# Kernel tuning notes

Measured on AMD Instinct MI355X. Metric: run time of the kernel, lower is better.

## Reference

```python
import jax, jax.numpy as jnp
import numpy as np

DIM = 1024
HEADS = 16
DIM_HEAD = 64
INNER = HEADS * DIM_HEAD
EPS_NORM = 1e-12  # F.normalize eps
LN_EPS = 1e-5     # torch F.layer_norm default eps


def setup_inputs() -> dict:
    key = jax.random.key(0)
    ks = jax.random.split(key, 6)
    x = jax.random.normal(ks[0], (8, 1024, DIM), dtype=jnp.float32)
    ln_gamma = jnp.ones((DIM,), jnp.float32)
    q_gamma = jnp.ones((HEADS, 1, DIM_HEAD), jnp.float32)
    k_gamma = jnp.ones((HEADS, 1, DIM_HEAD), jnp.float32)
    # nn.Linear default init ~ U(-1/sqrt(fan_in), 1/sqrt(fan_in))
    w_qkv = jax.random.uniform(ks[1], (DIM, 3 * INNER), jnp.float32, -1.0, 1.0) / np.sqrt(DIM)
    w_out = jax.random.uniform(ks[2], (INNER, DIM), jnp.float32, -1.0, 1.0) / np.sqrt(INNER)
    return {"x": x, "ln_gamma": ln_gamma, "q_gamma": q_gamma, "k_gamma": k_gamma,
            "w_qkv": w_qkv, "w_out": w_out}


def _layer_norm(x, gamma):
    mu = jnp.mean(x, axis=-1, keepdims=True)
    var = jnp.var(x, axis=-1, keepdims=True)
    return (x - mu) * jax.lax.rsqrt(var + LN_EPS) * gamma  # beta is zeros buffer


def _rms(x, gamma):
    # F.normalize(x, dim=-1) * sqrt(d) * gamma
    n = jnp.linalg.norm(x, axis=-1, keepdims=True)
    normed = x / jnp.maximum(n, EPS_NORM)
    return normed * (DIM_HEAD ** 0.5) * gamma


def reference(x, ln_gamma, q_gamma, k_gamma, w_qkv, w_out):
    b, n, _ = x.shape
    h, d = HEADS, DIM_HEAD
    xn = _layer_norm(x, ln_gamma)
    qkv = xn @ w_qkv  # [b, n, 3*inner]
    q, k, v = jnp.split(qkv, 3, axis=-1)
    # b n (h d) -> b h n d
    to_heads = lambda t: t.reshape(b, n, h, d).transpose(0, 2, 1, 3)
    q, k, v = to_heads(q), to_heads(k), to_heads(v)
    q = _rms(q, q_gamma)
    k = _rms(k, k_gamma)
    dots = jnp.einsum('bhid,bhjd->bhij', q, k)  # no extra scale (scale baked into RMSNorm)
    attn = jax.nn.softmax(dots, axis=-1)
    out = jnp.einsum('bhij,bhjd->bhid', attn, v)
    out = out.transpose(0, 2, 1, 3).reshape(b, n, h * d)
    return out @ w_out
```

## Files before the change

### kernel.cpp

```cpp
#include <hip/hip_runtime.h>
#include <hip/hip_bf16.h>
#include <math.h>

#define DIMX   1024
#define HEADS  16
#define DH     64
#define NB     8
#define NSEQ   1024
#define ROWS   (NB * NSEQ)
#define QKVW   (3 * DIMX)

typedef _Float16 half8 __attribute__((ext_vector_type(8)));
typedef _Float16 half4 __attribute__((ext_vector_type(4)));
typedef float floatx4 __attribute__((ext_vector_type(4)));

#define GLD_LDS16(gptr, lptr) __builtin_amdgcn_global_load_lds( \
    (const __attribute__((address_space(1))) void*)(gptr),      \
    (__attribute__((address_space(3))) void*)(lptr), 16, 0, 0)

__global__ __launch_bounds__(256) void ln_kernel(const float* __restrict__ x,
                                                 const float* __restrict__ gamma,
                                                 _Float16* __restrict__ xn) {
    int row = blockIdx.x;
    const float* xr = x + (size_t)row * DIMX;
    _Float16* xo = xn + (size_t)row * DIMX;
    int t = threadIdx.x;

    float4 v = ((const float4*)xr)[t];
    float s  = v.x + v.y + v.z + v.w;
    float ss = v.x*v.x + v.y*v.y + v.z*v.z + v.w*v.w;

    #pragma unroll
    for (int o = 32; o > 0; o >>= 1) {
        s  += __shfl_down(s, o);
        ss += __shfl_down(ss, o);
    }
    __shared__ float sbuf[4], ssbuf[4];
    int lane = t & 63, wid = t >> 6;
    if (lane == 0) { sbuf[wid] = s; ssbuf[wid] = ss; }
    __syncthreads();
    if (t == 0) {
        float a = 0.f, b2 = 0.f;
        for (int i = 0; i < 4; i++) { a += sbuf[i]; b2 += ssbuf[i]; }
        sbuf[0] = a; ssbuf[0] = b2;
    }
    __syncthreads();
    float mean = sbuf[0] * (1.0f / DIMX);
    float var  = ssbuf[0] * (1.0f / DIMX) - mean * mean;
    float rstd = rsqrtf(var + 1e-5f);

    float4 g = ((const float4*)gamma)[t];
    half4 o;
    o.x = (_Float16)((v.x - mean) * rstd * g.x);
    o.y = (_Float16)((v.y - mean) * rstd * g.y);
    o.z = (_Float16)((v.z - mean) * rstd * g.z);
    o.w = (_Float16)((v.w - mean) * rstd * g.w);
    *(half4*)(xo + t * 4) = o;
}

__global__ __launch_bounds__(256) void wtrans(const float* __restrict__ W,
                                              _Float16* __restrict__ WT,
                                              int K, int N) {
    __shared__ float tile[32][33];
    int n0 = blockIdx.x * 32, k0 = blockIdx.y * 32;
    int tx = threadIdx.x & 31, ty = threadIdx.x >> 5;
    #pragma unroll
    for (int i = 0; i < 32; i += 8)
        tile[ty + i][tx] = W[(size_t)(k0 + ty + i) * N + n0 + tx];
    __syncthreads();
    #pragma unroll
    for (int i = 0; i < 32; i += 8)
        WT[(size_t)(n0 + ty + i) * K + k0 + tx] = (_Float16)tile[tx][ty + i];
}

template <typename CT>
__global__ __launch_bounds__(256) void hgemm(const _Float16* __restrict__ A,
                                             const _Float16* __restrict__ BT,
                                             CT* __restrict__ C,
                                             int M, int N, int K) {
    __shared__ _Float16 As[128 * 64];
    __shared__ _Float16 Bs[128 * 64];

    int t = threadIdx.x;
    int wave = t >> 6, lane = t & 63;
    int quad = lane >> 4, l16 = lane & 15;
    int wm = (wave >> 1) * 64, wn = (wave & 1) * 64;
    size_t m0 = (size_t)blockIdx.y * 128, n0 = (size_t)blockIdx.x * 128;

    floatx4 acc[4][4] = {};

    int sr = t >> 3, sg = t & 7;
    int swz = sg ^ (sr & 7);
    const _Float16* ag = A  + (m0 + sr) * (size_t)K + swz * 8;
    const _Float16* bg = BT + (n0 + sr) * (size_t)K + swz * 8;
    char* lA = (char*)As + (t >> 6) * 1024;
    char* lB = (char*)Bs + (t >> 6) * 1024;

    for (int k0 = 0; k0 < K; k0 += 64) {
        #pragma unroll
        for (int i = 0; i < 4; i++) {
            GLD_LDS16(ag + (size_t)(i * 32) * K + k0, lA + i * 4096);
            GLD_LDS16(bg + (size_t)(i * 32) * K + k0, lB + i * 4096);
        }
        __syncthreads();

        half8 af[2][4], bf[2][4];
        #pragma unroll
        for (int kk = 0; kk < 2; kk++) {
            #pragma unroll
            for (int mf = 0; mf < 4; mf++)
                af[kk][mf] = *(const half8*)&As[(wm + mf * 16 + l16) * 64
                                 + (((kk * 4 + quad) ^ (l16 & 7)) * 8)];
            #pragma unroll
            for (int nf = 0; nf < 4; nf++)
                bf[kk][nf] = *(const half8*)&Bs[(wn + nf * 16 + l16) * 64
                                 + (((kk * 4 + quad) ^ (l16 & 7)) * 8)];
        }

        #pragma unroll
        for (int kk = 0; kk < 2; kk++)
            #pragma unroll
            for (int mf = 0; mf < 4; mf++)
                #pragma unroll
                for (int nf = 0; nf < 4; nf++)
                    acc[mf][nf] = __builtin_amdgcn_mfma_f32_16x16x32_f16(
                        af[kk][mf], bf[kk][nf], acc[mf][nf], 0, 0, 0);
        __syncthreads();
    }

    #pragma unroll
    for (int mf = 0; mf < 4; mf++)
        #pragma unroll
        for (int nf = 0; nf < 4; nf++)
            #pragma unroll
            for (int r = 0; r < 4; r++) {
                size_t row = m0 + wm + mf * 16 + quad * 4 + r;
                size_t col = n0 + wn + nf * 16 + l16;
                C[row * N + col] = (CT)acc[mf][nf][r];
            }
}

__global__ __launch_bounds__(256) void rmsvt(const _Float16* __restrict__ qkv,
                                             const float* __restrict__ qg,
                                             const float* __restrict__ kg,
                                             _Float16* __restrict__ qf,
                                             _Float16* __restrict__ kf,
                                             _Float16* __restrict__ vt) {
    __shared__ _Float16 tile[64][72];
    int blk = blockIdx.x;
    int bh = blk >> 4, nt = blk & 15;
    int b = bh >> 4, h = bh & 15;
    int t = threadIdx.x;
    int r = t >> 2, cg = t & 3;

    const _Float16* src = qkv + ((size_t)(b * NSEQ) + nt * 64 + r) * QKVW + h * 64 + cg * 16;
    size_t drow = ((size_t)bh * 1024 + nt * 64 + r) * 64 + cg * 16;

    half8 q0 = *(const half8*)(src);
    half8 q1 = *(const half8*)(src + 8);
    float sq = 0.f;
    #pragma unroll
    for (int j = 0; j < 8; j++) { float a=(float)q0[j], b2=(float)q1[j]; sq += a*a + b2*b2; }
    sq += __shfl_xor(sq, 1); sq += __shfl_xor(sq, 2);
    float qs = 8.0f / fmaxf(sqrtf(sq), 1e-12f);
    half8 oq0, oq1;
    #pragma unroll
    for (int j = 0; j < 8; j++) {
        oq0[j] = (_Float16)((float)q0[j] * qs * qg[h * 64 + cg * 16 + j]);
        oq1[j] = (_Float16)((float)q1[j] * qs * qg[h * 64 + cg * 16 + 8 + j]);
    }
    *(half8*)(qf + drow) = oq0;
    *(half8*)(qf + drow + 8) = oq1;

    half8 k0 = *(const half8*)(src + DIMX);
    half8 k1 = *(const half8*)(src + DIMX + 8);
    float sk = 0.f;
    #pragma unroll
    for (int j = 0; j < 8; j++) { float a=(float)k0[j], b2=(float)k1[j]; sk += a*a + b2*b2; }
    sk += __shfl_xor(sk, 1); sk += __shfl_xor(sk, 2);
    float ks = 8.0f / fmaxf(sqrtf(sk), 1e-12f);
    half8 ok0, ok1;
    #pragma unroll
    for (int j = 0; j < 8; j++) {
        ok0[j] = (_Float16)((float)k0[j] * ks * kg[h * 64 + cg * 16 + j]);
        ok1[j] = (_Float16)((float)k1[j] * ks * kg[h * 64 + cg * 16 + 8 + j]);
    }
    *(half8*)(kf + drow) = ok0;
    *(half8*)(kf + drow + 8) = ok1;

    half8 v0 = *(const half8*)(src + 2 * DIMX);
    half8 v1 = *(const half8*)(src + 2 * DIMX + 8);
    #pragma unroll
    for (int j = 0; j < 8; j++) tile[cg * 16 + j][r] = v0[j];
    #pragma unroll
    for (int j = 0; j < 8; j++) tile[cg * 16 + 8 + j][r] = v1[j];
    __syncthreads();
    int d = t >> 2, ng = t & 3;
    half8 w0, w1;
    #pragma unroll
    for (int j = 0; j < 8; j++) { w0[j] = tile[d][ng * 16 + j]; w1[j] = tile[d][ng * 16 + 8 + j]; }
    _Float16* vdst = vt + ((size_t)blk * 64 + d) * 64 + ng * 16;
    *(half8*)vdst = w0;
    *(half8*)(vdst + 8) = w1;
}

__global__ __launch_bounds__(256) void flash_kernel(const _Float16* __restrict__ qf,
                                                    const _Float16* __restrict__ kf,
                                                    const _Float16* __restrict__ vt,
                                                    _Float16* __restrict__ obuf) {
    __shared__ _Float16 Ks[64 * 64];
    __shared__ _Float16 VTs[64 * 64];
    __shared__ _Float16 Ps[4][16][72];

    int t = threadIdx.x;
    int wave = t >> 6, lane = t & 63;
    int quad = lane >> 4, l16 = lane & 15;
    int bh = blockIdx.x >> 3, qt = blockIdx.x & 7;

    const _Float16* qb = qf + ((size_t)bh * 1024 + qt * 128) * 64;
    const _Float16* kb = kf + (size_t)bh * 65536;
    const _Float16* vb = vt + (size_t)bh * 65536;

    half8 aq[2][2];
    #pragma unroll
    for (int st = 0; st < 2; st++) {
        const _Float16* qrow = qb + (wave * 32 + st * 16 + l16) * 64;
        aq[st][0] = *(const half8*)(qrow + quad * 8);
        aq[st][1] = *(const half8*)(qrow + 32 + quad * 8);
    }

    floatx4 o[2][4] = {};
    float m_i[2] = {-INFINITY, -INFINITY};
    float l_i[2] = {0.f, 0.f};

    int sr = t >> 3;
    int sg = t & 7;
    int swz = sg ^ (sr & 7);
    char* lK = (char*)Ks  + (t >> 6) * 1024;
    char* lV = (char*)VTs + (t >> 6) * 1024;

    for (int kt = 0; kt < 16; kt++) {
        const _Float16* kbt = kb + (size_t)kt * 64 * 64;
        const _Float16* vbt = vb + (size_t)kt * 64 * 64;
        #pragma unroll
        for (int i = 0; i < 2; i++) {
            GLD_LDS16(kbt + (i * 32 + sr) * 64 + swz * 8, lK + i * 4096);
            GLD_LDS16(vbt + (i * 32 + sr) * 64 + swz * 8, lV + i * 4096);
        }
        __syncthreads();

        #pragma unroll
        for (int st = 0; st < 2; st++) {
            floatx4 sc[4] = {};
            #pragma unroll
            for (int kc = 0; kc < 2; kc++) {
                #pragma unroll
                for (int nf = 0; nf < 4; nf++) {
                    half8 ak = *(const half8*)&Ks[(nf * 16 + l16) * 64
                                    + (((kc * 4 + quad) ^ (l16 & 7)) * 8)];
                    sc[nf] = __builtin_amdgcn_mfma_f32_16x16x32_f16(
                        ak, aq[st][kc], sc[nf], 0, 0, 0);
                }
            }

            float mx = sc[0][0];
            #pragma unroll
            for (int nf = 0; nf < 4; nf++)
                #pragma unroll
                for (int r = 0; r < 4; r++) mx = fmaxf(mx, sc[nf][r]);
            mx = fmaxf(mx, __shfl_xor(mx, 16));
            mx = fmaxf(mx, __shfl_xor(mx, 32));
            float mnew = fmaxf(m_i[st], mx);
            float alpha = __expf(m_i[st] - mnew);
            m_i[st] = mnew;
            float psum = 0.f;
            #pragma unroll
            for (int nf = 0; nf < 4; nf++)
                #pragma unroll
                for (int r = 0; r < 4; r++) {
                    float p = __expf(sc[nf][r] - mnew);
                    sc[nf][r] = p;
                    psum += p;
                }
            l_i[st] = l_i[st] * alpha + psum;
            #pragma unroll
            for (int nf = 0; nf < 4; nf++) o[st][nf] *= alpha;

            #pragma unroll
            for (int nf = 0; nf < 4; nf++) {
                half4 p4;
                #pragma unroll
                for (int r = 0; r < 4; r++) p4[r] = (_Float16)sc[nf][r];
                *(half4*)&Ps[wave][l16][nf * 16 + quad * 4] = p4;
            }

            #pragma unroll
            for (int kc = 0; kc < 2; kc++) {
                half8 bp = *(const half8*)&Ps[wave][l16][kc * 32 + quad * 8];
                #pragma unroll
                for (int nf = 0; nf < 4; nf++) {
                    half8 av = *(const half8*)&VTs[(nf * 16 + l16) * 64
                                    + (((kc * 4 + quad) ^ (l16 & 7)) * 8)];
                    o[st][nf] = __builtin_amdgcn_mfma_f32_16x16x32_f16(
                        av, bp, o[st][nf], 0, 0, 0);
                }
            }
        }
        __syncthreads();
    }

    int b = bh >> 4, h = bh & 15;
    #pragma unroll
    for (int st = 0; st < 2; st++) {
        float lsum = l_i[st];
        lsum += __shfl_xor(lsum, 16);
        lsum += __shfl_xor(lsum, 32);
        float inv = 1.0f / lsum;
        size_t row = (size_t)b * NSEQ + qt * 128 + wave * 32 + st * 16 + l16;
        #pragma unroll
        for (int nf = 0; nf < 4; nf++) {
            half4 o4;
            #pragma unroll
            for (int r = 0; r < 4; r++) o4[r] = (_Float16)(o[st][nf][r] * inv);
            *(half4*)(obuf + row * 1024 + h * 64 + nf * 16 + quad * 4) = o4;
        }
    }
}

extern "C" void kernel_launch(void* const* d_in, const int* in_sizes, int n_in,
                              void* d_out, int out_size, void* d_ws, size_t ws_size,
                              hipStream_t stream) {
    const float* x     = (const float*)d_in[0];
    const float* ln_g  = (const float*)d_in[1];
    const float* q_g   = (const float*)d_in[2];
    const float* k_g   = (const float*)d_in[3];
    const float* w_qkv = (const float*)d_in[4];
    const float* w_out = (const float*)d_in[5];
    float* out = (float*)d_out;

    char* base = (char*)d_ws;
    _Float16* xn    = (_Float16*)(base);
    _Float16* obuf  = (_Float16*)(base);
    _Float16* qkv   = (_Float16*)(base + (16ull << 20));
    _Float16* wqkvT = (_Float16*)(base + (64ull << 20));
    _Float16* woutT = (_Float16*)(base + (72ull << 20));
    _Float16* qf    = (_Float16*)(base + (80ull << 20));
    _Float16* kf    = (_Float16*)(base + (96ull << 20));
    _Float16* vt    = (_Float16*)(base + (112ull << 20));

    ln_kernel<<<ROWS, 256, 0, stream>>>(x, ln_g, xn);

    dim3 gt1(QKVW / 32, DIMX / 32);
    wtrans<<<gt1, 256, 0, stream>>>(w_qkv, wqkvT, DIMX, QKVW);

    dim3 g1(QKVW / 128, ROWS / 128);
    hgemm<_Float16><<<g1, 256, 0, stream>>>(xn, wqkvT, qkv, ROWS, QKVW, DIMX);

    rmsvt<<<NB * HEADS * (NSEQ / 64), 256, 0, stream>>>(qkv, q_g, k_g, qf, kf, vt);

    dim3 gt2(DIMX / 32, DIMX / 32);
    wtrans<<<gt2, 256, 0, stream>>>(w_out, woutT, DIMX, DIMX);

    flash_kernel<<<NB * HEADS * (NSEQ / 128), 256, 0, stream>>>(qf, kf, vt, obuf);

    dim3 g2(DIMX / 128, ROWS / 128);
    hgemm<float><<<g2, 256, 0, stream>>>(obuf, woutT, out, ROWS, DIMX, DIMX);
}
```

Before: 288.7 us.

## Fuse q/k RMS norm into QKV GEMM epilogue, merge weight transposes, use exp2 softmax

The QKV GEMM now swaps its MFMA operands so each lane holds a token row, and applies the q/k RMS normalization and head-major scatter in its epilogue. This removes the full fp16 qkv buffer round trip and the separate rmsvt pass. Only a small V-transpose kernel remains. The two weight transposes are merged into one launch, and the softmax switches to exp2 with log2e folded into q, rescaling lazily only when the row max grows. The output GEMM writes float4 vectors, and the P staging buffer padding is changed. The cost is more register pressure in the GEMM epilogue and divergent branches in the softmax.

```diff
diff --git a/kernel.cpp b/kernel.cpp
--- a/kernel.cpp
+++ b/kernel.cpp
@@ -9,6 +9,7 @@
 #define NSEQ   1024
 #define ROWS   (NB * NSEQ)
 #define QKVW   (3 * DIMX)
+#define LOG2E  1.44269504088896f
 
 typedef _Float16 half8 __attribute__((ext_vector_type(8)));
 typedef _Float16 half4 __attribute__((ext_vector_type(4)));
@@ -17,6 +18,14 @@
 #define GLD_LDS16(gptr, lptr) __builtin_amdgcn_global_load_lds( \
     (const __attribute__((address_space(1))) void*)(gptr),      \
     (__attribute__((address_space(3))) void*)(lptr), 16, 0, 0)
+
+__device__ __forceinline__ float fexp2(float x) {
+#if __has_builtin(__builtin_amdgcn_exp2f)
+    return __builtin_amdgcn_exp2f(x);
+#else
+    return __expf(x * 0.69314718056f);
+#endif
+}
 
 __global__ __launch_bounds__(256) void ln_kernel(const float* __restrict__ x,
                                                  const float* __restrict__ gamma,
@@ -58,11 +67,15 @@
     *(half4*)(xo + t * 4) = o;
 }
 
-__global__ __launch_bounds__(256) void wtrans(const float* __restrict__ W,
-                                              _Float16* __restrict__ WT,
-                                              int K, int N) {
+__global__ __launch_bounds__(256) void wtrans2(const float* __restrict__ Wq,
+                                               const float* __restrict__ Wo,
+                                               _Float16* __restrict__ WqT,
+                                               _Float16* __restrict__ WoT) {
     __shared__ float tile[32][33];
-    int n0 = blockIdx.x * 32, k0 = blockIdx.y * 32;
+    const float* W; _Float16* WT; int N, n0;
+    if (blockIdx.x < 96) { W = Wq; WT = WqT; N = QKVW; n0 = blockIdx.x * 32; }
+    else                 { W = Wo; WT = WoT; N = DIMX; n0 = (blockIdx.x - 96) * 32; }
+    int k0 = blockIdx.y * 32;
     int tx = threadIdx.x & 31, ty = threadIdx.x >> 5;
     #pragma unroll
     for (int i = 0; i < 32; i += 8)
@@ -70,21 +83,25 @@
     __syncthreads();
     #pragma unroll
     for (int i = 0; i < 32; i += 8)
-        WT[(size_t)(n0 + ty + i) * K + k0 + tx] = (_Float16)tile[tx][ty + i];
-}
-
-template <typename CT>
-__global__ __launch_bounds__(256) void hgemm(const _Float16* __restrict__ A,
-                                             const _Float16* __restrict__ BT,
-                                             CT* __restrict__ C,
-                                             int M, int N, int K) {
+        WT[(size_t)(n0 + ty + i) * 1024 + k0 + tx] = (_Float16)tile[tx][ty + i];
+}
+
+__global__ __launch_bounds__(256) void hgemm_qkv(const _Float16* __restrict__ A,
+                                                 const _Float16* __restrict__ BT,
+                                                 const float* __restrict__ qg,
+                                                 const float* __restrict__ kg,
+                                                 _Float16* __restrict__ qf,
+                                                 _Float16* __restrict__ kf,
+                                                 _Float16* __restrict__ vraw) {
     __shared__ _Float16 As[128 * 64];
     __shared__ _Float16 Bs[128 * 64];
+    const int K = DIMX;
 
     int t = threadIdx.x;
     int wave = t >> 6, lane = t & 63;
     int quad = lane >> 4, l16 = lane & 15;
-    int wm = (wave >> 1) * 64, wn = (wave & 1) * 64;
+    int wm = (wave >> 1) * 64;
+    int wn = (wave & 1) * 64;
     size_t m0 = (size_t)blockIdx.y * 128, n0 = (size_t)blockIdx.x * 128;
 
     floatx4 acc[4][4] = {};
@@ -124,72 +141,63 @@
                 #pragma unroll
                 for (int nf = 0; nf < 4; nf++)
                     acc[mf][nf] = __builtin_amdgcn_mfma_f32_16x16x32_f16(
-                        af[kk][mf], bf[kk][nf], acc[mf][nf], 0, 0, 0);
-        __syncthreads();
-    }
-
-    #pragma unroll
-    for (int mf = 0; mf < 4; mf++)
-        #pragma unroll
-        for (int nf = 0; nf < 4; nf++)
-            #pragma unroll
-            for (int r = 0; r < 4; r++) {
-                size_t row = m0 + wm + mf * 16 + quad * 4 + r;
-                size_t col = n0 + wn + nf * 16 + l16;
-                C[row * N + col] = (CT)acc[mf][nf][r];
-            }
-}
-
-__global__ __launch_bounds__(256) void rmsvt(const _Float16* __restrict__ qkv,
-                                             const float* __restrict__ qg,
-                                             const float* __restrict__ kg,
-                                             _Float16* __restrict__ qf,
-                                             _Float16* __restrict__ kf,
-                                             _Float16* __restrict__ vt) {
+                        bf[kk][nf], af[kk][mf], acc[mf][nf], 0, 0, 0);
+        __syncthreads();
+    }
+
+    int which = (int)(n0 >> 10);
+    int nloc  = ((int)n0 & 1023) + wn;
+    int h = nloc >> 6;
+    const float* g = (which == 0) ? qg : kg;
+    float emul = (which == 0) ? LOG2E : 1.0f;
+    _Float16* dstbuf = (which == 0) ? qf : (which == 1) ? kf : vraw;
+
+    #pragma unroll
+    for (int mf = 0; mf < 4; mf++) {
+        size_t tok = m0 + wm + mf * 16 + l16;
+        int b = (int)(tok >> 10), ntk = (int)(tok & 1023);
+        _Float16* dst = dstbuf + (((size_t)(b * 16 + h)) * 1024 + ntk) * 64;
+        if (which < 2) {
+            float ss = 0.f;
+            #pragma unroll
+            for (int nf = 0; nf < 4; nf++)
+                #pragma unroll
+                for (int r = 0; r < 4; r++) ss += acc[mf][nf][r] * acc[mf][nf][r];
+            ss += __shfl_xor(ss, 16);
+            ss += __shfl_xor(ss, 32);
+            float scale = 8.0f * emul / fmaxf(sqrtf(ss), 1e-12f);
+            #pragma unroll
+            for (int nf = 0; nf < 4; nf++) {
+                half4 p;
+                #pragma unroll
+                for (int r = 0; r < 4; r++)
+                    p[r] = (_Float16)(acc[mf][nf][r] * scale *
+                                      g[h * 64 + nf * 16 + quad * 4 + r]);
+                *(half4*)(dst + nf * 16 + quad * 4) = p;
+            }
+        } else {
+            #pragma unroll
+            for (int nf = 0; nf < 4; nf++) {
+                half4 p;
+                #pragma unroll
+                for (int r = 0; r < 4; r++) p[r] = (_Float16)acc[mf][nf][r];
+                *(half4*)(dst + nf * 16 + quad * 4) = p;
+            }
+        }
+    }
+}
+
+__global__ __launch_bounds__(256) void vtrans(const _Float16* __restrict__ vraw,
+                                              _Float16* __restrict__ vt) {
     __shared__ _Float16 tile[64][72];
     int blk = blockIdx.x;
     int bh = blk >> 4, nt = blk & 15;
-    int b = bh >> 4, h = bh & 15;
     int t = threadIdx.x;
     int r = t >> 2, cg = t & 3;
 
-    const _Float16* src = qkv + ((size_t)(b * NSEQ) + nt * 64 + r) * QKVW + h * 64 + cg * 16;
-    size_t drow = ((size_t)bh * 1024 + nt * 64 + r) * 64 + cg * 16;
-
-    half8 q0 = *(const half8*)(src);
-    half8 q1 = *(const half8*)(src + 8);
-    float sq = 0.f;
-    #pragma unroll
-    for (int j = 0; j < 8; j++) { float a=(float)q0[j], b2=(float)q1[j]; sq += a*a + b2*b2; }
-    sq += __shfl_xor(sq, 1); sq += __shfl_xor(sq, 2);
-    float qs = 8.0f / fmaxf(sqrtf(sq), 1e-12f);
-    half8 oq0, oq1;
-    #pragma unroll
-    for (int j = 0; j < 8; j++) {
-        oq0[j] = (_Float16)((float)q0[j] * qs * qg[h * 64 + cg * 16 + j]);
-        oq1[j] = (_Float16)((float)q1[j] * qs * qg[h * 64 + cg * 16 + 8 + j]);
-    }
-    *(half8*)(qf + drow) = oq0;
-    *(half8*)(qf + drow + 8) = oq1;
-
-    half8 k0 = *(const half8*)(src + DIMX);
-    half8 k1 = *(const half8*)(src + DIMX + 8);
-    float sk = 0.f;
-    #pragma unroll
-    for (int j = 0; j < 8; j++) { float a=(float)k0[j], b2=(float)k1[j]; sk += a*a + b2*b2; }
-    sk += __shfl_xor(sk, 1); sk += __shfl_xor(sk, 2);
-    float ks = 8.0f / fmaxf(sqrtf(sk), 1e-12f);
-    half8 ok0, ok1;
-    #pragma unroll
-    for (int j = 0; j < 8; j++) {
-        ok0[j] = (_Float16)((float)k0[j] * ks * kg[h * 64 + cg * 16 + j]);
-        ok1[j] = (_Float16)((float)k1[j] * ks * kg[h * 64 + cg * 16 + 8 + j]);
-    }
-    *(half8*)(kf + drow) = ok0;
-    *(half8*)(kf + drow + 8) = ok1;
-
-    half8 v0 = *(const half8*)(src + 2 * DIMX);
-    half8 v1 = *(const half8*)(src + 2 * DIMX + 8);
+    const _Float16* src = vraw + ((size_t)bh * 1024 + nt * 64 + r) * 64 + cg * 16;
+    half8 v0 = *(const half8*)src;
+    half8 v1 = *(const half8*)(src + 8);
     #pragma unroll
     for (int j = 0; j < 8; j++) tile[cg * 16 + j][r] = v0[j];
     #pragma unroll
@@ -210,7 +218,7 @@
                                                     _Float16* __restrict__ obuf) {
     __shared__ _Float16 Ks[64 * 64];
     __shared__ _Float16 VTs[64 * 64];
-    __shared__ _Float16 Ps[4][16][72];
+    __shared__ _Float16 Ps[4][16][68];
 
     int t = threadIdx.x;
     int wave = t >> 6, lane = t & 63;
@@ -270,21 +278,24 @@
                 for (int r = 0; r < 4; r++) mx = fmaxf(mx, sc[nf][r]);
             mx = fmaxf(mx, __shfl_xor(mx, 16));
             mx = fmaxf(mx, __shfl_xor(mx, 32));
-            float mnew = fmaxf(m_i[st], mx);
-            float alpha = __expf(m_i[st] - mnew);
-            m_i[st] = mnew;
+            if (mx > m_i[st]) {
+                float alpha = fexp2(m_i[st] - mx);
+                l_i[st] *= alpha;
+                #pragma unroll
+                for (int nf = 0; nf < 4; nf++) o[st][nf] *= alpha;
+                m_i[st] = mx;
+            }
+            float mcur = m_i[st];
             float psum = 0.f;
             #pragma unroll
             for (int nf = 0; nf < 4; nf++)
                 #pragma unroll
                 for (int r = 0; r < 4; r++) {
-                    float p = __expf(sc[nf][r] - mnew);
+                    float p = fexp2(sc[nf][r] - mcur);
                     sc[nf][r] = p;
                     psum += p;
                 }
-            l_i[st] = l_i[st] * alpha + psum;
-            #pragma unroll
-            for (int nf = 0; nf < 4; nf++) o[st][nf] *= alpha;
+            l_i[st] += psum;
 
             #pragma unroll
             for (int nf = 0; nf < 4; nf++) {
@@ -296,7 +307,11 @@
 
             #pragma unroll
             for (int kc = 0; kc < 2; kc++) {
-                half8 bp = *(const half8*)&Ps[wave][l16][kc * 32 + quad * 8];
+                half4 p0 = *(const half4*)&Ps[wave][l16][kc * 32 + quad * 8];
+                half4 p1 = *(const half4*)&Ps[wave][l16][kc * 32 + quad * 8 + 4];
+                half8 bp;
+                #pragma unroll
+                for (int j = 0; j < 4; j++) { bp[j] = p0[j]; bp[4 + j] = p1[j]; }
                 #pragma unroll
                 for (int nf = 0; nf < 4; nf++) {
                     half8 av = *(const half8*)&VTs[(nf * 16 + l16) * 64
@@ -324,6 +339,69 @@
             for (int r = 0; r < 4; r++) o4[r] = (_Float16)(o[st][nf][r] * inv);
             *(half4*)(obuf + row * 1024 + h * 64 + nf * 16 + quad * 4) = o4;
         }
+    }
+}
+
+__global__ __launch_bounds__(256) void hgemm_out(const _Float16* __restrict__ A,
+                                                 const _Float16* __restrict__ BT,
+                                                 float* __restrict__ C) {
+    __shared__ _Float16 As[128 * 64];
+    __shared__ _Float16 Bs[128 * 64];
+    const int K = DIMX, N = DIMX;
+
+    int t = threadIdx.x;
+    int wave = t >> 6, lane = t & 63;
+    int quad = lane >> 4, l16 = lane & 15;
+    int wm = (wave >> 1) * 64, wn = (wave & 1) * 64;
+    size_t m0 = (size_t)blockIdx.y * 128, n0 = (size_t)blockIdx.x * 128;
+
+    floatx4 acc[4][4] = {};
+
+    int sr = t >> 3, sg = t & 7;
+    int swz = sg ^ (sr & 7);
+    const _Float16* ag = A  + (m0 + sr) * (size_t)K + swz * 8;
+    const _Float16* bg = BT + (n0 + sr) * (size_t)K + swz * 8;
+    char* lA = (char*)As + (t >> 6) * 1024;
+    char* lB = (char*)Bs + (t >> 6) * 1024;
+
+    for (int k0 = 0; k0 < K; k0 += 64) {
+        #pragma unroll
+        for (int i = 0; i < 4; i++) {
+            GLD_LDS16(ag + (size_t)(i * 32) * K + k0, lA + i * 4096);
+            GLD_LDS16(bg + (size_t)(i * 32) * K + k0, lB + i * 4096);
+        }
+        __syncthreads();
+
+        half8 af[2][4], bf[2][4];
+        #pragma unroll
+        for (int kk = 0; kk < 2; kk++) {
+            #pragma unroll
+            for (int mf = 0; mf < 4; mf++)
+                af[kk][mf] = *(const half8*)&As[(wm + mf * 16 + l16) * 64
+                                 + (((kk * 4 + quad) ^ (l16 & 7)) * 8)];
+            #pragma unroll
+            for (int nf = 0; nf < 4; nf++)
+                bf[kk][nf] = *(const half8*)&Bs[(wn + nf * 16 + l16) * 64
+                                 + (((kk * 4 + quad) ^ (l16 & 7)) * 8)];
+        }
+
+        #pragma unroll
+        for (int kk = 0; kk < 2; kk++)
+            #pragma unroll
+            for (int mf = 0; mf < 4; mf++)
+                #pragma unroll
+                for (int nf = 0; nf < 4; nf++)
+                    acc[mf][nf] = __builtin_amdgcn_mfma_f32_16x16x32_f16(
+                        bf[kk][nf], af[kk][mf], acc[mf][nf], 0, 0, 0);
+        __syncthreads();
+    }
+
+    #pragma unroll
+    for (int mf = 0; mf < 4; mf++) {
+        size_t tok = m0 + wm + mf * 16 + l16;
+        #pragma unroll
+        for (int nf = 0; nf < 4; nf++)
+            *(floatx4*)(C + tok * N + n0 + wn + nf * 16 + quad * 4) = acc[mf][nf];
     }
 }
 
@@ -340,29 +418,26 @@
 
     char* base = (char*)d_ws;
     _Float16* xn    = (_Float16*)(base);
-    _Float16* obuf  = (_Float16*)(base);
-    _Float16* qkv   = (_Float16*)(base + (16ull << 20));
-    _Float16* wqkvT = (_Float16*)(base + (64ull << 20));
-    _Float16* woutT = (_Float16*)(base + (72ull << 20));
-    _Float16* qf    = (_Float16*)(base + (80ull << 20));
-    _Float16* kf    = (_Float16*)(base + (96ull << 20));
-    _Float16* vt    = (_Float16*)(base + (112ull << 20));
+    _Float16* wqkvT = (_Float16*)(base + (16ull << 20));
+    _Float16* woutT = (_Float16*)(base + (22ull << 20));
+    _Float16* qf    = (_Float16*)(base + (24ull << 20));
+    _Float16* kf    = (_Float16*)(base + (40ull << 20));
+    _Float16* vraw  = (_Float16*)(base + (56ull << 20));
+    _Float16* vt    = (_Float16*)(base + (72ull << 20));
+    _Float16* obuf  = (_Float16*)(base + (88ull << 20));
 
     ln_kernel<<<ROWS, 256, 0, stream>>>(x, ln_g, xn);
 
-    dim3 gt1(QKVW / 32, DIMX / 32);
-    wtrans<<<gt1, 256, 0, stream>>>(w_qkv, wqkvT, DIMX, QKVW);
+    dim3 gt(128, 32);
+    wtrans2<<<gt, 256, 0, stream>>>(w_qkv, w_out, wqkvT, woutT);
 
     dim3 g1(QKVW / 128, ROWS / 128);
-    hgemm<_Float16><<<g1, 256, 0, stream>>>(xn, wqkvT, qkv, ROWS, QKVW, DIMX);
-
-    rmsvt<<<NB * HEADS * (NSEQ / 64), 256, 0, stream>>>(qkv, q_g, k_g, qf, kf, vt);
-
-    dim3 gt2(DIMX / 32, DIMX / 32);
-    wtrans<<<gt2, 256, 0, stream>>>(w_out, woutT, DIMX, DIMX);
+    hgemm_qkv<<<g1, 256, 0, stream>>>(xn, wqkvT, q_g, k_g, qf, kf, vraw);
+
+    vtrans<<<NB * HEADS * (NSEQ / 64), 256, 0, stream>>>(vraw, vt);
 
     flash_kernel<<<NB * HEADS * (NSEQ / 128), 256, 0, stream>>>(qf, kf, vt, obuf);
 
     dim3 g2(DIMX / 128, ROWS / 128);
-    hgemm<float><<<g2, 256, 0, stream>>>(obuf, woutT, out, ROWS, DIMX, DIMX);
-}
+    hgemm_out<<<g2, 256, 0, stream>>>(obuf, woutT, out);
+}
```

Result: faster. 270.6 us (-6.2%).
